# Optimization experiments

Measured on AMD Instinct MI355X. Metric: run time of the kernel, lower is better.

## Reference

```python
import jax, jax.numpy as jnp
import numpy as np

B, SEQ, EMB, HID = 256, 256, 128, 512
NG = 1          # n_glimpses
CEXP = 10.0     # tanh_exploration
NEG = -1e9      # masked-logit value (stands in for -inf)


def setup_inputs():
    key = jax.random.key(0)
    ks = jax.random.split(key, 19)
    se = 1.0 / np.sqrt(EMB)
    sh = 1.0 / np.sqrt(HID)
    u = lambda k, shape, s: jax.random.uniform(k, shape, jnp.float32, -s, s)
    return {
        'embedding': u(ks[0], (SEQ, EMB), 1.0),
        'enc_Wih': u(ks[1], (4 * HID, EMB), sh),
        'enc_Whh': u(ks[2], (4 * HID, HID), sh),
        'enc_b': u(ks[3], (4 * HID,), sh),
        'dec_Wih': u(ks[4], (4 * HID, EMB), sh),
        'dec_Whh': u(ks[5], (4 * HID, HID), sh),
        'dec_b': u(ks[6], (4 * HID,), sh),
        'pt_Wq': u(ks[7], (HID, HID), sh), 'pt_bq': u(ks[8], (HID,), sh),
        'pt_Wref': u(ks[9], (HID, HID), sh), 'pt_bref': u(ks[10], (HID,), sh),
        'pt_V': u(ks[11], (HID,), sh),
        'gl_Wq': u(ks[12], (HID, HID), sh), 'gl_bq': u(ks[13], (HID,), sh),
        'gl_Wref': u(ks[14], (HID, HID), sh), 'gl_bref': u(ks[15], (HID,), sh),
        'gl_V': u(ks[16], (HID,), sh),
        'dec_start': u(ks[17], (EMB,), se),
        'inputs': jax.random.randint(ks[18], (B, SEQ), 0, SEQ),
    }


def lstm_cell(x, h, c, Wih, Whh, b):
    # PyTorch gate order: i, f, g, o
    g = x @ Wih.T + h @ Whh.T + b
    i, f, gg, o = jnp.split(g, 4, axis=1)
    c = jax.nn.sigmoid(f) * c + jax.nn.sigmoid(i) * jnp.tanh(gg)
    h = jax.nn.sigmoid(o) * jnp.tanh(c)
    return h, c


def reference(embedding, enc_Wih, enc_Whh, enc_b,
              dec_Wih, dec_Whh, dec_b,
              pt_Wq, pt_bq, pt_Wref, pt_bref, pt_V,
              gl_Wq, gl_bq, gl_Wref, gl_bref, gl_V,
              dec_start, inputs):
    emb = embedding[inputs]                      # [B,S,E]
    h0 = jnp.zeros((B, HID), jnp.float32)
    c0 = jnp.zeros((B, HID), jnp.float32)

    def enc_step(carry, x_t):
        h, c = carry
        h, c = lstm_cell(x_t, h, c, enc_Wih, enc_Whh, enc_b)
        return (h, c), h

    (h, c), hs = jax.lax.scan(enc_step, (h0, c0), jnp.swapaxes(emb, 0, 1))
    enc_out = jnp.swapaxes(hs, 0, 1)             # [B,S,H]

    # W_ref is a 1x1 Conv1d == per-position linear; precompute once (constant across steps)
    gl_ref = enc_out @ gl_Wref.T + gl_bref       # [B,S,H]
    pt_ref = enc_out @ pt_Wref.T + pt_bref       # [B,S,H]

    keys = jax.random.split(jax.random.key(1), SEQ)
    mask0 = jnp.zeros((B, SEQ), bool)
    dec_in0 = jnp.broadcast_to(dec_start, (B, EMB))

    def dec_step(carry, key_i):
        h, c, mask, dec_in = carry
        h, c = lstm_cell(dec_in, h, c, dec_Wih, dec_Whh, dec_b)
        q = h                                    # [B,H]
        for _ in range(NG):
            gl = jnp.tanh((q @ gl_Wq.T + gl_bq)[:, None, :] + gl_ref) @ gl_V  # [B,S]
            gl = jnp.where(mask, NEG, gl)
            q = jnp.einsum('bsh,bs->bh', gl_ref, jax.nn.softmax(gl, axis=1))
        lg = jnp.tanh((q @ pt_Wq.T + pt_bq)[:, None, :] + pt_ref) @ pt_V      # [B,S]
        lg = CEXP * jnp.tanh(lg)                 # use_tanh=True pointer
        lg = jnp.where(mask, NEG, lg)
        # Categorical sample via Gumbel-max
        gum = -jnp.log(-jnp.log(jax.random.uniform(key_i, (B, SEQ)) + 1e-10) + 1e-10)
        ptr = jnp.argmax(lg + gum, axis=1)       # [B]
        logp = jnp.take_along_axis(jax.nn.log_softmax(lg, axis=1), ptr[:, None], axis=1)[:, 0]
        mask = mask.at[jnp.arange(B), ptr].set(True)
        dec_in = emb[jnp.arange(B), ptr]         # embedding of chosen city
        return (h, c, mask, dec_in), (ptr, logp)

    _, (tours, logps) = jax.lax.scan(dec_step, (h, c, mask0, dec_in0), keys)
    return jnp.swapaxes(tours, 0, 1), jnp.swapaxes(logps, 0, 1)  # [B,S] each
```

## Files before the change

### kernel.cpp

```cpp
#include <hip/hip_runtime.h>
#include <math.h>


#define Bz 256
#define Sz 256
#define Ez 128
#define Hz 512
#define NEGV -1e9f
#define BH (Bz*Hz)

__device__ float g_encout[Bz*Sz*Hz];
__device__ float g_glref[Bz*Sz*Hz];
__device__ float g_ptref[Bz*Sz*Hz];
__device__ float g_xpe[256*2048];
__device__ float g_xpd[257*2048];
__device__ float g_h[2*BH];
__device__ float g_c[BH];
__device__ int g_ptrbuf[Bz];
__device__ unsigned g_keys[2*Sz];
__device__ unsigned char g_mask[Bz*Sz];

__device__ __forceinline__ unsigned rotl32(unsigned v, int d){ return (v<<d)|(v>>(32-d)); }

__device__ __forceinline__ void tf2x32(unsigned k0, unsigned k1, unsigned x0, unsigned x1,
                                       unsigned &o0, unsigned &o1){
  unsigned ks2 = k0 ^ k1 ^ 0x1BD11BDAu;
  x0 += k0; x1 += k1;
#define TFR(r) { x0 += x1; x1 = rotl32(x1,(r)); x1 ^= x0; }
  TFR(13) TFR(15) TFR(26) TFR(6)
  x0 += k1; x1 += ks2 + 1u;
  TFR(17) TFR(29) TFR(16) TFR(24)
  x0 += ks2; x1 += k0 + 2u;
  TFR(13) TFR(15) TFR(26) TFR(6)
  x0 += k0; x1 += k1 + 3u;
  TFR(17) TFR(29) TFR(16) TFR(24)
  x0 += k1; x1 += ks2 + 4u;
  TFR(13) TFR(15) TFR(26) TFR(6)
  x0 += ks2; x1 += k0 + 5u;
#undef TFR
  o0 = x0; o1 = x1;
}

__device__ __forceinline__ unsigned rng_bits(unsigned ka, unsigned kb, unsigned idx){
  unsigned o0,o1; tf2x32(ka,kb, 0u, idx, o0,o1);
  return o0 ^ o1;
}

__global__ __launch_bounds__(256) void init_kernel(){
  int i = blockIdx.x*256 + threadIdx.x;
  if (i < BH){ g_h[i] = 0.f; g_c[i] = 0.f; }
  if (i < Bz*Sz) g_mask[i] = 0;
  if (i < Sz){
    unsigned o0,o1; tf2x32(0u,1u, 0u, (unsigned)i, o0,o1);
    g_keys[2*i] = o0; g_keys[2*i+1] = o1;
  }
}

__global__ __launch_bounds__(256) void xproj_kernel(
    const float* __restrict__ Wih, const float* __restrict__ bias,
    const float* __restrict__ emb, const float* __restrict__ dstart,
    int dst)
{
  float* Xp = dst ? g_xpd : g_xpe;
  int c = blockIdx.x;
  int row = blockIdx.y*256 + threadIdx.x;
  __shared__ float xs[Ez];
  if (threadIdx.x < Ez) xs[threadIdx.x] = (c < 256) ? emb[c*Ez + threadIdx.x]
                                                    : dstart[threadIdx.x];
  __syncthreads();
  float a = bias[row];
  const float* w = Wih + (size_t)row*Ez;
  #pragma unroll 8
  for (int k = 0; k < Ez; k++) a = fmaf(xs[k], w[k], a);
  Xp[(size_t)c*2048 + row] = a;
}

__global__ __launch_bounds__(256) void lstm_step(
    const float* __restrict__ Whh,
    const int*   __restrict__ inputs,
    int t, int is_dec, int hsel)
{
  __shared__ float A_lds[32][36];
  __shared__ float W_lds[64][36];

  const float* h_in = g_h + (size_t)hsel*BH;
  float*       h_out = g_h + (size_t)(hsel^1)*BH;
  const float* Xp = is_dec ? g_xpd : g_xpe;

  int tid = threadIdx.x;
  int bt = blockIdx.x;
  int jt = blockIdx.y;
  int jj = tid & 15;
  int bp = tid >> 4;
  int jglob = jt*16 + jj;

  int bA = bt*32 + bp*2, bB = bA + 1;
  int cA, cB;
  if (is_dec){
    if (t == 0){ cA = 256; cB = 256; }
    else { cA = inputs[bA*Sz + g_ptrbuf[bA]]; cB = inputs[bB*Sz + g_ptrbuf[bB]]; }
  } else {
    cA = inputs[bA*Sz + t]; cB = inputs[bB*Sz + t];
  }

  float acc[2][4];
  {
    const float* xa = Xp + (size_t)cA*2048;
    const float* xb = Xp + (size_t)cB*2048;
    #pragma unroll
    for (int g=0; g<4; g++){
      acc[0][g] = xa[g*Hz + jglob];
      acc[1][g] = xb[g*Hz + jglob];
    }
  }

  int sr = tid >> 3;
  int sk = (tid & 7) * 4;
  int wr = tid >> 2;
  int wk = (tid & 3) * 8;
  int bg = bt*32 + sr;
  int wrow_g = (wr >> 4)*Hz + jt*16 + (wr & 15);

  for (int kc = 0; kc < 16; kc++){
    int k0 = kc*32;
    __syncthreads();
    {
      float4 av = *(const float4*)(h_in + (size_t)bg*Hz + k0 + sk);
      *(float4*)&A_lds[sr][sk] = av;
    }
    {
      const float* ws = Whh + (size_t)wrow_g*Hz + k0 + wk;
      float4 w0 = *(const float4*)ws;
      float4 w1 = *(const float4*)(ws + 4);
      *(float4*)&W_lds[wr][wk]     = w0;
      *(float4*)&W_lds[wr][wk + 4] = w1;
    }
    __syncthreads();
    #pragma unroll
    for (int k4 = 0; k4 < 8; k4++){
      float4 w0 = *(const float4*)&W_lds[jj      ][k4*4];
      float4 w1 = *(const float4*)&W_lds[16 + jj ][k4*4];
      float4 w2 = *(const float4*)&W_lds[32 + jj ][k4*4];
      float4 w3 = *(const float4*)&W_lds[48 + jj ][k4*4];
      float4 a0 = *(const float4*)&A_lds[bp*2    ][k4*4];
      float4 a1 = *(const float4*)&A_lds[bp*2 + 1][k4*4];
#define LSTEP(c) \
      acc[0][0]=fmaf(a0.c,w0.c,acc[0][0]); acc[0][1]=fmaf(a0.c,w1.c,acc[0][1]); \
      acc[0][2]=fmaf(a0.c,w2.c,acc[0][2]); acc[0][3]=fmaf(a0.c,w3.c,acc[0][3]); \
      acc[1][0]=fmaf(a1.c,w0.c,acc[1][0]); acc[1][1]=fmaf(a1.c,w1.c,acc[1][1]); \
      acc[1][2]=fmaf(a1.c,w2.c,acc[1][2]); acc[1][3]=fmaf(a1.c,w3.c,acc[1][3]);
      LSTEP(x) LSTEP(y) LSTEP(z) LSTEP(w)
#undef LSTEP
    }
  }

  #pragma unroll
  for (int r=0;r<2;r++){
    int b = bA + r;
    float gi = acc[r][0], gf = acc[r][1], gg = acc[r][2], go = acc[r][3];
    float co = g_c[(size_t)b*Hz + jglob];
    float si = 1.f/(1.f + expf(-gi));
    float sf = 1.f/(1.f + expf(-gf));
    float so = 1.f/(1.f + expf(-go));
    float cn = sf*co + si*tanhf(gg);
    float hn = so*tanhf(cn);
    g_c[(size_t)b*Hz + jglob] = cn;
    h_out[(size_t)b*Hz + jglob] = hn;
    if (!is_dec) g_encout[((size_t)b*Sz + t)*Hz + jglob] = hn;
  }
}

__global__ __launch_bounds__(256) void gemm_ref(
    const float* __restrict__ W, const float* __restrict__ bias, int dst_id)
{
  const float* A = g_encout;
  float*       C = (dst_id == 1) ? g_glref : g_ptref;
  __shared__ float As[32][68];
  __shared__ float Ws[32][68];
  int tid = threadIdx.x;
  int mt = blockIdx.x * 64, nt = blockIdx.y * 64;
  int tm = (tid & 15) * 4, tn = (tid >> 4) * 4;
  float acc[4][4] = {};
  int lr = tid >> 2;
  int lk = (tid & 3) * 8;

  for (int kc = 0; kc < 16; kc++){
    int k0 = kc*32;
    __syncthreads();
    {
      const float* ar = A + (size_t)(mt + lr)*Hz + k0 + lk;
      float4 a0 = *(const float4*)ar, a1 = *(const float4*)(ar+4);
      As[lk+0][lr]=a0.x; As[lk+1][lr]=a0.y; As[lk+2][lr]=a0.z; As[lk+3][lr]=a0.w;
      As[lk+4][lr]=a1.x; As[lk+5][lr]=a1.y; As[lk+6][lr]=a1.z; As[lk+7][lr]=a1.w;
      const float* wrp = W + (size_t)(nt + lr)*Hz + k0 + lk;
      float4 w0 = *(const float4*)wrp, w1 = *(const float4*)(wrp+4);
      Ws[lk+0][lr]=w0.x; Ws[lk+1][lr]=w0.y; Ws[lk+2][lr]=w0.z; Ws[lk+3][lr]=w0.w;
      Ws[lk+4][lr]=w1.x; Ws[lk+5][lr]=w1.y; Ws[lk+6][lr]=w1.z; Ws[lk+7][lr]=w1.w;
    }
    __syncthreads();
    #pragma unroll
    for (int k=0;k<32;k++){
      float4 av = *(const float4*)&As[k][tm];
      float4 wv = *(const float4*)&Ws[k][tn];
      acc[0][0]=fmaf(av.x,wv.x,acc[0][0]); acc[0][1]=fmaf(av.x,wv.y,acc[0][1]);
      acc[0][2]=fmaf(av.x,wv.z,acc[0][2]); acc[0][3]=fmaf(av.x,wv.w,acc[0][3]);
      acc[1][0]=fmaf(av.y,wv.x,acc[1][0]); acc[1][1]=fmaf(av.y,wv.y,acc[1][1]);
      acc[1][2]=fmaf(av.y,wv.z,acc[1][2]); acc[1][3]=fmaf(av.y,wv.w,acc[1][3]);
      acc[2][0]=fmaf(av.z,wv.x,acc[2][0]); acc[2][1]=fmaf(av.z,wv.y,acc[2][1]);
      acc[2][2]=fmaf(av.z,wv.z,acc[2][2]); acc[2][3]=fmaf(av.z,wv.w,acc[2][3]);
      acc[3][0]=fmaf(av.w,wv.x,acc[3][0]); acc[3][1]=fmaf(av.w,wv.y,acc[3][1]);
      acc[3][2]=fmaf(av.w,wv.z,acc[3][2]); acc[3][3]=fmaf(av.w,wv.w,acc[3][3]);
    }
  }
  float b0v = bias[nt+tn+0], b1v = bias[nt+tn+1], b2v = bias[nt+tn+2], b3v = bias[nt+tn+3];
  #pragma unroll
  for (int i=0;i<4;i++){
    float4 o;
    o.x = acc[i][0] + b0v; o.y = acc[i][1] + b1v;
    o.z = acc[i][2] + b2v; o.w = acc[i][3] + b3v;
    *(float4*)(C + (size_t)(mt + tm + i)*Hz + nt + tn) = o;
  }
}

__global__ __launch_bounds__(512) void attn_step(
    const float* __restrict__ gl_Wq, const float* __restrict__ gl_bq,
    const float* __restrict__ gl_V,
    const float* __restrict__ pt_Wq, const float* __restrict__ pt_bq,
    const float* __restrict__ pt_V,
    int t, int hsel2, float* __restrict__ out)
{
  int b = blockIdx.x, tid = threadIdx.x;
  int wave = tid >> 6, lane64 = tid & 63;
  int g = tid >> 5, lane = tid & 31;

  __shared__ __align__(16) float hq[Hz];
  __shared__ __align__(16) float q2s[Hz];
  __shared__ __align__(16) float qgs[Hz];
  __shared__ __align__(16) float qps[Hz];
  __shared__ __align__(16) float vgl[Hz];
  __shared__ __align__(16) float vpt[Hz];
  __shared__ float part[16][513];
  __shared__ float m_arr[16];
  __shared__ float l_arr[16];
  __shared__ int   rlist[16][16];
  __shared__ float slog[Sz];
  __shared__ float redy[8]; __shared__ int redi[8];
  __shared__ float redm[8]; __shared__ float redsum[8];

  hq[tid]  = g_h[(size_t)hsel2*BH + (size_t)b*Hz + tid];
  vgl[tid] = gl_V[tid];
  vpt[tid] = pt_V[tid];
  __syncthreads();

  const unsigned char* mrow = g_mask + b*Sz;

  int cnt;
  {
    bool un = (lane < 16) ? (mrow[g*16 + lane] == 0) : false;
    unsigned long long bal = __ballot(un);
    unsigned m16 = (unsigned)((g & 1) ? (bal >> 32) : bal) & 0xFFFFu;
    cnt = __popc(m16);
    if (lane < 16){
      if (un){
        int rank = __popc(m16 & ((1u << lane) - 1u));
        rlist[g][rank] = g*16 + lane;
      } else {
        slog[g*16 + lane] = NEGV;
      }
    }
  }

  {
    float hv[8];
    #pragma unroll
    for (int i=0;i<8;i++) hv[i] = hq[lane64*8 + i];
    for (int jj=0;jj<64;jj+=2){
      int j0 = wave*64 + jj;
      const float* wr0 = gl_Wq + (size_t)j0*Hz + lane64*8;
      const float* wr1 = wr0 + Hz;
      float4 A0 = *(const float4*)wr0, A1 = *(const float4*)(wr0+4);
      float4 B0 = *(const float4*)wr1, B1 = *(const float4*)(wr1+4);
      float p0 = 0.f, p1 = 0.f;
      p0 = fmaf(hv[0], A0.x, p0); p0 = fmaf(hv[1], A0.y, p0);
      p0 = fmaf(hv[2], A0.z, p0); p0 = fmaf(hv[3], A0.w, p0);
      p0 = fmaf(hv[4], A1.x, p0); p0 = fmaf(hv[5], A1.y, p0);
      p0 = fmaf(hv[6], A1.z, p0); p0 = fmaf(hv[7], A1.w, p0);
      p1 = fmaf(hv[0], B0.x, p1); p1 = fmaf(hv[1], B0.y, p1);
      p1 = fmaf(hv[2], B0.z, p1); p1 = fmaf(hv[3], B0.w, p1);
      p1 = fmaf(hv[4], B1.x, p1); p1 = fmaf(hv[5], B1.y, p1);
      p1 = fmaf(hv[6], B1.z, p1); p1 = fmaf(hv[7], B1.w, p1);
      #pragma unroll
      for (int off=32; off; off>>=1) p0 += __shfl_xor(p0, off);
      #pragma unroll
      for (int off=32; off; off>>=1) p1 += __shfl_xor(p1, off);
      if (lane64 == 0){ q2s[j0] = p0 + gl_bq[j0]; q2s[j0+1] = p1 + gl_bq[j0+1]; }
    }
  }
  __syncthreads();

  const float* glbase = g_glref + (size_t)b*Sz*Hz;
  {
    float m_g = -INFINITY, l_g = 0.f;
    float4 racc[4];
    { float4 z = {0.f,0.f,0.f,0.f}; racc[0]=z; racc[1]=z; racc[2]=z; racc[3]=z; }

    float4 xn0, xn1, xn2, xn3;
    if (cnt > 0){
      const float4* rp = (const float4*)(glbase + (size_t)rlist[g][0]*Hz);
      xn0 = rp[lane]; xn1 = rp[lane+32]; xn2 = rp[lane+64]; xn3 = rp[lane+96];
    }
    for (int i = 0; i < cnt; i++){
      float4 x0 = xn0, x1 = xn1, x2 = xn2, x3 = xn3;
      if (i + 1 < cnt){
        const float4* rp = (const float4*)(glbase + (size_t)rlist[g][i+1]*Hz);
        xn0 = rp[lane]; xn1 = rp[lane+32]; xn2 = rp[lane+64]; xn3 = rp[lane+96];
      }
      float p = 0.f;
      {
        float4 q, vv;
        q = *(const float4*)&q2s[lane*4];        vv = *(const float4*)&vgl[lane*4];
        p = fmaf(vv.x, tanhf(q.x + x0.x), p); p = fmaf(vv.y, tanhf(q.y + x0.y), p);
        p = fmaf(vv.z, tanhf(q.z + x0.z), p); p = fmaf(vv.w, tanhf(q.w + x0.w), p);
        q = *(const float4*)&q2s[(lane+32)*4];   vv = *(const float4*)&vgl[(lane+32)*4];
        p = fmaf(vv.x, tanhf(q.x + x1.x), p); p = fmaf(vv.y, tanhf(q.y + x1.y), p);
        p = fmaf(vv.z, tanhf(q.z + x1.z), p); p = fmaf(vv.w, tanhf(q.w + x1.w), p);
        q = *(const float4*)&q2s[(lane+64)*4];   vv = *(const float4*)&vgl[(lane+64)*4];
        p = fmaf(vv.x, tanhf(q.x + x2.x), p); p = fmaf(vv.y, tanhf(q.y + x2.y), p);
        p = fmaf(vv.z, tanhf(q.z + x2.z), p); p = fmaf(vv.w, tanhf(q.w + x2.w), p);
        q = *(const float4*)&q2s[(lane+96)*4];   vv = *(const float4*)&vgl[(lane+96)*4];
        p = fmaf(vv.x, tanhf(q.x + x3.x), p); p = fmaf(vv.y, tanhf(q.y + x3.y), p);
        p = fmaf(vv.z, tanhf(q.z + x3.z), p); p = fmaf(vv.w, tanhf(q.w + x3.w), p);
      }
      #pragma unroll
      for (int off=16; off; off>>=1) p += __shfl_xor(p, off, 32);
      float lgv = p;
      if (lgv > m_g){
        float r_ = expf(m_g - lgv);
        l_g *= r_;
        racc[0].x*=r_; racc[0].y*=r_; racc[0].z*=r_; racc[0].w*=r_;
        racc[1].x*=r_; racc[1].y*=r_; racc[1].z*=r_; racc[1].w*=r_;
        racc[2].x*=r_; racc[2].y*=r_; racc[2].z*=r_; racc[2].w*=r_;
        racc[3].x*=r_; racc[3].y*=r_; racc[3].z*=r_; racc[3].w*=r_;
        m_g = lgv;
      }
      float pr = expf(lgv - m_g);
      l_g += pr;
      racc[0].x=fmaf(pr,x0.x,racc[0].x); racc[0].y=fmaf(pr,x0.y,racc[0].y);
      racc[0].z=fmaf(pr,x0.z,racc[0].z); racc[0].w=fmaf(pr,x0.w,racc[0].w);
      racc[1].x=fmaf(pr,x1.x,racc[1].x); racc[1].y=fmaf(pr,x1.y,racc[1].y);
      racc[1].z=fmaf(pr,x1.z,racc[1].z); racc[1].w=fmaf(pr,x1.w,racc[1].w);
      racc[2].x=fmaf(pr,x2.x,racc[2].x); racc[2].y=fmaf(pr,x2.y,racc[2].y);
      racc[2].z=fmaf(pr,x2.z,racc[2].z); racc[2].w=fmaf(pr,x2.w,racc[2].w);
      racc[3].x=fmaf(pr,x3.x,racc[3].x); racc[3].y=fmaf(pr,x3.y,racc[3].y);
      racc[3].z=fmaf(pr,x3.z,racc[3].z); racc[3].w=fmaf(pr,x3.w,racc[3].w);
    }
    if (lane == 0){ m_arr[g] = m_g; l_arr[g] = l_g; }
    part[g][4*lane+  0] = racc[0].x; part[g][4*lane+  1] = racc[0].y;
    part[g][4*lane+  2] = racc[0].z; part[g][4*lane+  3] = racc[0].w;
    part[g][4*lane+128] = racc[1].x; part[g][4*lane+129] = racc[1].y;
    part[g][4*lane+130] = racc[1].z; part[g][4*lane+131] = racc[1].w;
    part[g][4*lane+256] = racc[2].x; part[g][4*lane+257] = racc[2].y;
    part[g][4*lane+258] = racc[2].z; part[g][4*lane+259] = racc[2].w;
    part[g][4*lane+384] = racc[3].x; part[g][4*lane+385] = racc[3].y;
    part[g][4*lane+386] = racc[3].z; part[g][4*lane+387] = racc[3].w;
  }
  __syncthreads();

  {
    float M = m_arr[0];
    #pragma unroll
    for (int gg=1; gg<16; gg++) M = fmaxf(M, m_arr[gg]);
    float num = 0.f, den = 0.f;
    #pragma unroll
    for (int gg=0; gg<16; gg++){
      float w = expf(m_arr[gg] - M);
      num = fmaf(w, part[gg][tid], num);
      den = fmaf(w, l_arr[gg], den);
    }
    qgs[tid] = num / den;
  }
  __syncthreads();

  {
    float qv[8];
    #pragma unroll
    for (int i=0;i<8;i++) qv[i] = qgs[lane64*8 + i];
    for (int jj=0;jj<64;jj+=2){
      int j0 = wave*64 + jj;
      const float* wr0 = pt_Wq + (size_t)j0*Hz + lane64*8;
      const float* wr1 = wr0 + Hz;
      float4 A0 = *(const float4*)wr0, A1 = *(const float4*)(wr0+4);
      float4 B0 = *(const float4*)wr1, B1 = *(const float4*)(wr1+4);
      float p0 = 0.f, p1 = 0.f;
      p0 = fmaf(qv[0], A0.x, p0); p0 = fmaf(qv[1], A0.y, p0);
      p0 = fmaf(qv[2], A0.z, p0); p0 = fmaf(qv[3], A0.w, p0);
      p0 = fmaf(qv[4], A1.x, p0); p0 = fmaf(qv[5], A1.y, p0);
      p0 = fmaf(qv[6], A1.z, p0); p0 = fmaf(qv[7], A1.w, p0);
      p1 = fmaf(qv[0], B0.x, p1); p1 = fmaf(qv[1], B0.y, p1);
      p1 = fmaf(qv[2], B0.z, p1); p1 = fmaf(qv[3], B0.w, p1);
      p1 = fmaf(qv[4], B1.x, p1); p1 = fmaf(qv[5], B1.y, p1);
      p1 = fmaf(qv[6], B1.z, p1); p1 = fmaf(qv[7], B1.w, p1);
      #pragma unroll
      for (int off=32; off; off>>=1) p0 += __shfl_xor(p0, off);
      #pragma unroll
      for (int off=32; off; off>>=1) p1 += __shfl_xor(p1, off);
      if (lane64 == 0){ qps[j0] = p0 + pt_bq[j0]; qps[j0+1] = p1 + pt_bq[j0+1]; }
    }
  }
  __syncthreads();

  const float* ptbase = g_ptref + (size_t)b*Sz*Hz;
  {
    float4 xn0, xn1, xn2, xn3;
    if (cnt > 0){
      const float4* rp = (const float4*)(ptbase + (size_t)rlist[g][0]*Hz);
      xn0 = rp[lane]; xn1 = rp[lane+32]; xn2 = rp[lane+64]; xn3 = rp[lane+96];
    }
    for (int i = 0; i < cnt; i++){
      int s = rlist[g][i];
      float4 x0 = xn0, x1 = xn1, x2 = xn2, x3 = xn3;
      if (i + 1 < cnt){
        const float4* rp = (const float4*)(ptbase + (size_t)rlist[g][i+1]*Hz);
        xn0 = rp[lane]; xn1 = rp[lane+32]; xn2 = rp[lane+64]; xn3 = rp[lane+96];
      }
      float p = 0.f;
      {
        float4 q, vv;
        q = *(const float4*)&qps[lane*4];        vv = *(const float4*)&vpt[lane*4];
        p = fmaf(vv.x, tanhf(q.x + x0.x), p); p = fmaf(vv.y, tanhf(q.y + x0.y), p);
        p = fmaf(vv.z, tanhf(q.z + x0.z), p); p = fmaf(vv.w, tanhf(q.w + x0.w), p);
        q = *(const float4*)&qps[(lane+32)*4];   vv = *(const float4*)&vpt[(lane+32)*4];
        p = fmaf(vv.x, tanhf(q.x + x1.x), p); p = fmaf(vv.y, tanhf(q.y + x1.y), p);
        p = fmaf(vv.z, tanhf(q.z + x1.z), p); p = fmaf(vv.w, tanhf(q.w + x1.w), p);
        q = *(const float4*)&qps[(lane+64)*4];   vv = *(const float4*)&vpt[(lane+64)*4];
        p = fmaf(vv.x, tanhf(q.x + x2.x), p); p = fmaf(vv.y, tanhf(q.y + x2.y), p);
        p = fmaf(vv.z, tanhf(q.z + x2.z), p); p = fmaf(vv.w, tanhf(q.w + x2.w), p);
        q = *(const float4*)&qps[(lane+96)*4];   vv = *(const float4*)&vpt[(lane+96)*4];
        p = fmaf(vv.x, tanhf(q.x + x3.x), p); p = fmaf(vv.y, tanhf(q.y + x3.y), p);
        p = fmaf(vv.z, tanhf(q.z + x3.z), p); p = fmaf(vv.w, tanhf(q.w + x3.w), p);
      }
      #pragma unroll
      for (int off=16; off; off>>=1) p += __shfl_xor(p, off, 32);
      if (lane == 0) slog[s] = 10.f * tanhf(p);
    }
  }
  __syncthreads();

  float lg = NEGV, y = -INFINITY;
  if (tid < Sz){
    lg = slog[tid];
    unsigned bits = rng_bits(g_keys[2*t], g_keys[2*t+1], (unsigned)(b*Sz + tid));
    float u = __uint_as_float((bits >> 9) | 0x3f800000u) - 1.f;
    float gum = -logf(-logf(u + 1e-10f) + 1e-10f);
    y = lg + gum;
  }
  float by = y; int bi = tid; float bm = lg;
  #pragma unroll
  for (int off=32; off; off>>=1){
    float oy = __shfl_xor(by, off);
    int   oi = __shfl_xor(bi, off);
    float om = __shfl_xor(bm, off);
    if (oy > by || (oy == by && oi < bi)){ by = oy; bi = oi; }
    bm = fmaxf(bm, om);
  }
  if (lane64 == 0){ redy[wave] = by; redi[wave] = bi; redm[wave] = bm; }
  __syncthreads();
  float fy = redy[0]; int fi = redi[0]; float fm = redm[0];
  #pragma unroll
  for (int w=1; w<8; w++){
    if (redy[w] > fy || (redy[w] == fy && redi[w] < fi)){ fy = redy[w]; fi = redi[w]; }
    fm = fmaxf(fm, redm[w]);
  }
  int ptr = fi;

  float pe = (tid < Sz) ? expf(lg - fm) : 0.f;
  #pragma unroll
  for (int off=32; off; off>>=1) pe += __shfl_xor(pe, off);
  if (lane64 == 0) redsum[wave] = pe;
  __syncthreads();
  if (tid == 0){
    float den = ((redsum[0]+redsum[1]) + (redsum[2]+redsum[3]))
              + ((redsum[4]+redsum[5]) + (redsum[6]+redsum[7]));
    float logp = slog[ptr] - fm - logf(den);
    out[(size_t)b*Sz + t] = (float)ptr;
    out[(size_t)Bz*Sz + (size_t)b*Sz + t] = logp;
    g_mask[b*Sz + ptr] = 1;
    g_ptrbuf[b] = ptr;
  }
}

extern "C" void kernel_launch(void* const* d_in, const int* in_sizes, int n_in,
                              void* d_out, int out_size, void* d_ws, size_t ws_size,
                              hipStream_t stream){
  (void)in_sizes; (void)n_in; (void)out_size; (void)d_ws; (void)ws_size;
  const float* embedding = (const float*)d_in[0];
  const float* enc_Wih = (const float*)d_in[1];
  const float* enc_Whh = (const float*)d_in[2];
  const float* enc_b   = (const float*)d_in[3];
  const float* dec_Wih = (const float*)d_in[4];
  const float* dec_Whh = (const float*)d_in[5];
  const float* dec_b   = (const float*)d_in[6];
  const float* pt_Wq   = (const float*)d_in[7];
  const float* pt_bq   = (const float*)d_in[8];
  const float* pt_Wref = (const float*)d_in[9];
  const float* pt_bref = (const float*)d_in[10];
  const float* pt_V    = (const float*)d_in[11];
  const float* gl_Wq   = (const float*)d_in[12];
  const float* gl_bq   = (const float*)d_in[13];
  const float* gl_Wref = (const float*)d_in[14];
  const float* gl_bref = (const float*)d_in[15];
  const float* gl_V    = (const float*)d_in[16];
  const float* dec_start = (const float*)d_in[17];
  const int*   inputs  = (const int*)d_in[18];
  float* out = (float*)d_out;

  init_kernel<<<512, 256, 0, stream>>>();
  xproj_kernel<<<dim3(256,8), 256, 0, stream>>>(enc_Wih, enc_b, embedding, dec_start, 0);
  xproj_kernel<<<dim3(257,8), 256, 0, stream>>>(dec_Wih, dec_b, embedding, dec_start, 1);

  for (int t = 0; t < Sz; t++){
    lstm_step<<<dim3(8,32), 256, 0, stream>>>(enc_Whh, inputs, t, 0, t & 1);
  }
  gemm_ref<<<dim3(1024,8), 256, 0, stream>>>(gl_Wref, gl_bref, 1);
  gemm_ref<<<dim3(1024,8), 256, 0, stream>>>(pt_Wref, pt_bref, 2);

  for (int t = 0; t < Sz; t++){
    lstm_step<<<dim3(8,32), 256, 0, stream>>>(dec_Whh, inputs, t, 1, t & 1);
    attn_step<<<Bz, 512, 0, stream>>>(gl_Wq, gl_bq, gl_V,
        pt_Wq, pt_bq, pt_V, t, (t+1) & 1, out);
  }
}
```

Before: 34.79 ms.

## Fuse whole rollout into one persistent cooperative kernel with grid syncs

Replaces the roughly 770 separate kernel launches (init, input projections, per-step encoder and decoder LSTM, reference GEMMs, per-step attention) with one cooperative kernel of 256 blocks × 512 threads. Phases are separated by grid.sync instead of kernel boundaries, and shared memory is held in a union across phases. The LSTM and GEMM tiles are reshaped so each thread in the larger 512-thread block does half the previous work. The aim is to remove per-launch overhead on the sequential recurrence. The cost is grid-wide barrier latency, higher register pressure from one monolithic kernel, and a fixed one-block-per-CU occupancy.

```diff
diff --git a/kernel.cpp b/kernel.cpp
--- a/kernel.cpp
+++ b/kernel.cpp
@@ -1,5 +1,8 @@
 #include <hip/hip_runtime.h>
+#include <hip/hip_cooperative_groups.h>
 #include <math.h>
+
+namespace cg = cooperative_groups;
 
 
 #define Bz 256
@@ -46,210 +49,141 @@
   return o0 ^ o1;
 }
 
-__global__ __launch_bounds__(256) void init_kernel(){
-  int i = blockIdx.x*256 + threadIdx.x;
-  if (i < BH){ g_h[i] = 0.f; g_c[i] = 0.f; }
-  if (i < Bz*Sz) g_mask[i] = 0;
-  if (i < Sz){
-    unsigned o0,o1; tf2x32(0u,1u, 0u, (unsigned)i, o0,o1);
-    g_keys[2*i] = o0; g_keys[2*i+1] = o1;
-  }
-}
-
-__global__ __launch_bounds__(256) void xproj_kernel(
-    const float* __restrict__ Wih, const float* __restrict__ bias,
-    const float* __restrict__ emb, const float* __restrict__ dstart,
-    int dst)
+struct AttnS {
+  float hq[Hz], q2s[Hz], qgs[Hz], qps[Hz], vgl[Hz], vpt[Hz];
+  float part[16][513];
+  float m_arr[16], l_arr[16];
+  int   rlist[16][16];
+  float slog[Sz];
+  float redy[8]; int redi[8]; float redm[8]; float redsum[8];
+};
+struct LstmS { float A[32][36]; float W[64][36]; };
+struct GemmS { float As[32][68]; float Ws[32][68]; };
+struct XprojS { float xs[Ez]; };
+union __align__(16) SharedU { AttnS a; LstmS l; GemmS g; XprojS x; };
+
+__device__ void lstm_phase(LstmS& S, const float* __restrict__ Whh,
+                           const int* __restrict__ inputs,
+                           int t, int is_dec, int hsel, int blk, int tid)
 {
-  float* Xp = dst ? g_xpd : g_xpe;
-  int c = blockIdx.x;
-  int row = blockIdx.y*256 + threadIdx.x;
-  __shared__ float xs[Ez];
-  if (threadIdx.x < Ez) xs[threadIdx.x] = (c < 256) ? emb[c*Ez + threadIdx.x]
-                                                    : dstart[threadIdx.x];
-  __syncthreads();
-  float a = bias[row];
-  const float* w = Wih + (size_t)row*Ez;
-  #pragma unroll 8
-  for (int k = 0; k < Ez; k++) a = fmaf(xs[k], w[k], a);
-  Xp[(size_t)c*2048 + row] = a;
-}
-
-__global__ __launch_bounds__(256) void lstm_step(
-    const float* __restrict__ Whh,
-    const int*   __restrict__ inputs,
-    int t, int is_dec, int hsel)
-{
-  __shared__ float A_lds[32][36];
-  __shared__ float W_lds[64][36];
-
-  const float* h_in = g_h + (size_t)hsel*BH;
+  const float* h_in  = g_h + (size_t)hsel*BH;
   float*       h_out = g_h + (size_t)(hsel^1)*BH;
   const float* Xp = is_dec ? g_xpd : g_xpe;
 
-  int tid = threadIdx.x;
-  int bt = blockIdx.x;
-  int jt = blockIdx.y;
-  int jj = tid & 15;
-  int bp = tid >> 4;
+  int bt = blk >> 5, jt = blk & 31;
+  int jj = tid & 15, bp = tid >> 4;
   int jglob = jt*16 + jj;
-
-  int bA = bt*32 + bp*2, bB = bA + 1;
-  int cA, cB;
-  if (is_dec){
-    if (t == 0){ cA = 256; cB = 256; }
-    else { cA = inputs[bA*Sz + g_ptrbuf[bA]]; cB = inputs[bB*Sz + g_ptrbuf[bB]]; }
-  } else {
-    cA = inputs[bA*Sz + t]; cB = inputs[bB*Sz + t];
-  }
-
-  float acc[2][4];
-  {
-    const float* xa = Xp + (size_t)cA*2048;
-    const float* xb = Xp + (size_t)cB*2048;
-    #pragma unroll
-    for (int g=0; g<4; g++){
-      acc[0][g] = xa[g*Hz + jglob];
-      acc[1][g] = xb[g*Hz + jglob];
-    }
-  }
-
-  int sr = tid >> 3;
+  int b = bt*32 + bp;
+
+  int c;
+  if (is_dec) c = (t == 0) ? 256 : inputs[b*Sz + g_ptrbuf[b]];
+  else        c = inputs[b*Sz + t];
+
+  float acc[4];
+  {
+    const float* xa = Xp + (size_t)c*2048;
+    #pragma unroll
+    for (int g=0; g<4; g++) acc[g] = xa[g*Hz + jglob];
+  }
+
   int sk = (tid & 7) * 4;
-  int wr = tid >> 2;
-  int wk = (tid & 3) * 8;
-  int bg = bt*32 + sr;
+  int wr = tid >> 3;
+  int bgA = bt*32 + (tid >> 3);
   int wrow_g = (wr >> 4)*Hz + jt*16 + (wr & 15);
 
   for (int kc = 0; kc < 16; kc++){
     int k0 = kc*32;
     __syncthreads();
+    if (tid < 256){
+      float4 av = *(const float4*)(h_in + (size_t)bgA*Hz + k0 + sk);
+      *(float4*)&S.A[tid>>3][sk] = av;
+    }
     {
-      float4 av = *(const float4*)(h_in + (size_t)bg*Hz + k0 + sk);
-      *(float4*)&A_lds[sr][sk] = av;
-    }
-    {
-      const float* ws = Whh + (size_t)wrow_g*Hz + k0 + wk;
+      const float* ws = Whh + (size_t)wrow_g*Hz + k0 + sk;
       float4 w0 = *(const float4*)ws;
-      float4 w1 = *(const float4*)(ws + 4);
-      *(float4*)&W_lds[wr][wk]     = w0;
-      *(float4*)&W_lds[wr][wk + 4] = w1;
+      *(float4*)&S.W[wr][sk] = w0;
     }
     __syncthreads();
     #pragma unroll
     for (int k4 = 0; k4 < 8; k4++){
-      float4 w0 = *(const float4*)&W_lds[jj      ][k4*4];
-      float4 w1 = *(const float4*)&W_lds[16 + jj ][k4*4];
-      float4 w2 = *(const float4*)&W_lds[32 + jj ][k4*4];
-      float4 w3 = *(const float4*)&W_lds[48 + jj ][k4*4];
-      float4 a0 = *(const float4*)&A_lds[bp*2    ][k4*4];
-      float4 a1 = *(const float4*)&A_lds[bp*2 + 1][k4*4];
-#define LSTEP(c) \
-      acc[0][0]=fmaf(a0.c,w0.c,acc[0][0]); acc[0][1]=fmaf(a0.c,w1.c,acc[0][1]); \
-      acc[0][2]=fmaf(a0.c,w2.c,acc[0][2]); acc[0][3]=fmaf(a0.c,w3.c,acc[0][3]); \
-      acc[1][0]=fmaf(a1.c,w0.c,acc[1][0]); acc[1][1]=fmaf(a1.c,w1.c,acc[1][1]); \
-      acc[1][2]=fmaf(a1.c,w2.c,acc[1][2]); acc[1][3]=fmaf(a1.c,w3.c,acc[1][3]);
+      float4 w0 = *(const float4*)&S.W[jj      ][k4*4];
+      float4 w1 = *(const float4*)&S.W[16 + jj ][k4*4];
+      float4 w2 = *(const float4*)&S.W[32 + jj ][k4*4];
+      float4 w3 = *(const float4*)&S.W[48 + jj ][k4*4];
+      float4 a0 = *(const float4*)&S.A[bp][k4*4];
+#define LSTEP(c_) \
+      acc[0]=fmaf(a0.c_,w0.c_,acc[0]); acc[1]=fmaf(a0.c_,w1.c_,acc[1]); \
+      acc[2]=fmaf(a0.c_,w2.c_,acc[2]); acc[3]=fmaf(a0.c_,w3.c_,acc[3]);
       LSTEP(x) LSTEP(y) LSTEP(z) LSTEP(w)
 #undef LSTEP
     }
   }
 
-  #pragma unroll
-  for (int r=0;r<2;r++){
-    int b = bA + r;
-    float gi = acc[r][0], gf = acc[r][1], gg = acc[r][2], go = acc[r][3];
-    float co = g_c[(size_t)b*Hz + jglob];
-    float si = 1.f/(1.f + expf(-gi));
-    float sf = 1.f/(1.f + expf(-gf));
-    float so = 1.f/(1.f + expf(-go));
-    float cn = sf*co + si*tanhf(gg);
-    float hn = so*tanhf(cn);
-    g_c[(size_t)b*Hz + jglob] = cn;
-    h_out[(size_t)b*Hz + jglob] = hn;
-    if (!is_dec) g_encout[((size_t)b*Sz + t)*Hz + jglob] = hn;
-  }
-}
-
-__global__ __launch_bounds__(256) void gemm_ref(
-    const float* __restrict__ W, const float* __restrict__ bias, int dst_id)
+  float gi = acc[0], gf = acc[1], gg = acc[2], go = acc[3];
+  float co = g_c[(size_t)b*Hz + jglob];
+  float si = 1.f/(1.f + expf(-gi));
+  float sf = 1.f/(1.f + expf(-gf));
+  float so = 1.f/(1.f + expf(-go));
+  float cn = sf*co + si*tanhf(gg);
+  float hn = so*tanhf(cn);
+  g_c[(size_t)b*Hz + jglob] = cn;
+  h_out[(size_t)b*Hz + jglob] = hn;
+  if (!is_dec) g_encout[((size_t)b*Sz + t)*Hz + jglob] = hn;
+}
+
+__device__ void gemm_tile(GemmS& S, const float* __restrict__ W,
+                          const float* __restrict__ bias, float* __restrict__ C,
+                          int mt, int nt, int tid)
 {
   const float* A = g_encout;
-  float*       C = (dst_id == 1) ? g_glref : g_ptref;
-  __shared__ float As[32][68];
-  __shared__ float Ws[32][68];
-  int tid = threadIdx.x;
-  int mt = blockIdx.x * 64, nt = blockIdx.y * 64;
-  int tm = (tid & 15) * 4, tn = (tid >> 4) * 4;
-  float acc[4][4] = {};
-  int lr = tid >> 2;
-  int lk = (tid & 3) * 8;
+  int tm = (tid & 15) * 4, tn = (tid >> 4) * 2;
+  float acc[4][2] = {};
+  int lr = tid >> 3;
+  int lk = (tid & 7) * 4;
 
   for (int kc = 0; kc < 16; kc++){
     int k0 = kc*32;
     __syncthreads();
     {
       const float* ar = A + (size_t)(mt + lr)*Hz + k0 + lk;
-      float4 a0 = *(const float4*)ar, a1 = *(const float4*)(ar+4);
-      As[lk+0][lr]=a0.x; As[lk+1][lr]=a0.y; As[lk+2][lr]=a0.z; As[lk+3][lr]=a0.w;
-      As[lk+4][lr]=a1.x; As[lk+5][lr]=a1.y; As[lk+6][lr]=a1.z; As[lk+7][lr]=a1.w;
+      float4 a0 = *(const float4*)ar;
+      S.As[lk+0][lr]=a0.x; S.As[lk+1][lr]=a0.y; S.As[lk+2][lr]=a0.z; S.As[lk+3][lr]=a0.w;
       const float* wrp = W + (size_t)(nt + lr)*Hz + k0 + lk;
-      float4 w0 = *(const float4*)wrp, w1 = *(const float4*)(wrp+4);
-      Ws[lk+0][lr]=w0.x; Ws[lk+1][lr]=w0.y; Ws[lk+2][lr]=w0.z; Ws[lk+3][lr]=w0.w;
-      Ws[lk+4][lr]=w1.x; Ws[lk+5][lr]=w1.y; Ws[lk+6][lr]=w1.z; Ws[lk+7][lr]=w1.w;
+      float4 w0 = *(const float4*)wrp;
+      S.Ws[lk+0][lr]=w0.x; S.Ws[lk+1][lr]=w0.y; S.Ws[lk+2][lr]=w0.z; S.Ws[lk+3][lr]=w0.w;
     }
     __syncthreads();
     #pragma unroll
     for (int k=0;k<32;k++){
-      float4 av = *(const float4*)&As[k][tm];
-      float4 wv = *(const float4*)&Ws[k][tn];
+      float4 av = *(const float4*)&S.As[k][tm];
+      float2 wv = *(const float2*)&S.Ws[k][tn];
       acc[0][0]=fmaf(av.x,wv.x,acc[0][0]); acc[0][1]=fmaf(av.x,wv.y,acc[0][1]);
-      acc[0][2]=fmaf(av.x,wv.z,acc[0][2]); acc[0][3]=fmaf(av.x,wv.w,acc[0][3]);
       acc[1][0]=fmaf(av.y,wv.x,acc[1][0]); acc[1][1]=fmaf(av.y,wv.y,acc[1][1]);
-      acc[1][2]=fmaf(av.y,wv.z,acc[1][2]); acc[1][3]=fmaf(av.y,wv.w,acc[1][3]);
       acc[2][0]=fmaf(av.z,wv.x,acc[2][0]); acc[2][1]=fmaf(av.z,wv.y,acc[2][1]);
-      acc[2][2]=fmaf(av.z,wv.z,acc[2][2]); acc[2][3]=fmaf(av.z,wv.w,acc[2][3]);
       acc[3][0]=fmaf(av.w,wv.x,acc[3][0]); acc[3][1]=fmaf(av.w,wv.y,acc[3][1]);
-      acc[3][2]=fmaf(av.w,wv.z,acc[3][2]); acc[3][3]=fmaf(av.w,wv.w,acc[3][3]);
-    }
-  }
-  float b0v = bias[nt+tn+0], b1v = bias[nt+tn+1], b2v = bias[nt+tn+2], b3v = bias[nt+tn+3];
+    }
+  }
+  float b0v = bias[nt+tn+0], b1v = bias[nt+tn+1];
   #pragma unroll
   for (int i=0;i<4;i++){
-    float4 o;
-    o.x = acc[i][0] + b0v; o.y = acc[i][1] + b1v;
-    o.z = acc[i][2] + b2v; o.w = acc[i][3] + b3v;
-    *(float4*)(C + (size_t)(mt + tm + i)*Hz + nt + tn) = o;
-  }
-}
-
-__global__ __launch_bounds__(512) void attn_step(
+    float2 o; o.x = acc[i][0] + b0v; o.y = acc[i][1] + b1v;
+    *(float2*)(C + (size_t)(mt + tm + i)*Hz + nt + tn) = o;
+  }
+}
+
+__device__ void attn_phase(AttnS& S,
     const float* __restrict__ gl_Wq, const float* __restrict__ gl_bq,
     const float* __restrict__ gl_V,
     const float* __restrict__ pt_Wq, const float* __restrict__ pt_bq,
     const float* __restrict__ pt_V,
-    int t, int hsel2, float* __restrict__ out)
+    int t, int hsel2, float* __restrict__ out, int b, int tid)
 {
-  int b = blockIdx.x, tid = threadIdx.x;
   int wave = tid >> 6, lane64 = tid & 63;
   int g = tid >> 5, lane = tid & 31;
 
-  __shared__ __align__(16) float hq[Hz];
-  __shared__ __align__(16) float q2s[Hz];
-  __shared__ __align__(16) float qgs[Hz];
-  __shared__ __align__(16) float qps[Hz];
-  __shared__ __align__(16) float vgl[Hz];
-  __shared__ __align__(16) float vpt[Hz];
-  __shared__ float part[16][513];
-  __shared__ float m_arr[16];
-  __shared__ float l_arr[16];
-  __shared__ int   rlist[16][16];
-  __shared__ float slog[Sz];
-  __shared__ float redy[8]; __shared__ int redi[8];
-  __shared__ float redm[8]; __shared__ float redsum[8];
-
-  hq[tid]  = g_h[(size_t)hsel2*BH + (size_t)b*Hz + tid];
-  vgl[tid] = gl_V[tid];
-  vpt[tid] = pt_V[tid];
+  S.hq[tid]  = g_h[(size_t)hsel2*BH + (size_t)b*Hz + tid];
+  S.vgl[tid] = gl_V[tid];
+  S.vpt[tid] = pt_V[tid];
   __syncthreads();
 
   const unsigned char* mrow = g_mask + b*Sz;
@@ -263,9 +197,9 @@
     if (lane < 16){
       if (un){
         int rank = __popc(m16 & ((1u << lane) - 1u));
-        rlist[g][rank] = g*16 + lane;
+        S.rlist[g][rank] = g*16 + lane;
       } else {
-        slog[g*16 + lane] = NEGV;
+        S.slog[g*16 + lane] = NEGV;
       }
     }
   }
@@ -273,7 +207,7 @@
   {
     float hv[8];
     #pragma unroll
-    for (int i=0;i<8;i++) hv[i] = hq[lane64*8 + i];
+    for (int i=0;i<8;i++) hv[i] = S.hq[lane64*8 + i];
     for (int jj=0;jj<64;jj+=2){
       int j0 = wave*64 + jj;
       const float* wr0 = gl_Wq + (size_t)j0*Hz + lane64*8;
@@ -293,7 +227,7 @@
       for (int off=32; off; off>>=1) p0 += __shfl_xor(p0, off);
       #pragma unroll
       for (int off=32; off; off>>=1) p1 += __shfl_xor(p1, off);
-      if (lane64 == 0){ q2s[j0] = p0 + gl_bq[j0]; q2s[j0+1] = p1 + gl_bq[j0+1]; }
+      if (lane64 == 0){ S.q2s[j0] = p0 + gl_bq[j0]; S.q2s[j0+1] = p1 + gl_bq[j0+1]; }
     }
   }
   __syncthreads();
@@ -306,28 +240,28 @@
 
     float4 xn0, xn1, xn2, xn3;
     if (cnt > 0){
-      const float4* rp = (const float4*)(glbase + (size_t)rlist[g][0]*Hz);
+      const float4* rp = (const float4*)(glbase + (size_t)S.rlist[g][0]*Hz);
       xn0 = rp[lane]; xn1 = rp[lane+32]; xn2 = rp[lane+64]; xn3 = rp[lane+96];
     }
     for (int i = 0; i < cnt; i++){
       float4 x0 = xn0, x1 = xn1, x2 = xn2, x3 = xn3;
       if (i + 1 < cnt){
-        const float4* rp = (const float4*)(glbase + (size_t)rlist[g][i+1]*Hz);
+        const float4* rp = (const float4*)(glbase + (size_t)S.rlist[g][i+1]*Hz);
         xn0 = rp[lane]; xn1 = rp[lane+32]; xn2 = rp[lane+64]; xn3 = rp[lane+96];
       }
       float p = 0.f;
       {
         float4 q, vv;
-        q = *(const float4*)&q2s[lane*4];        vv = *(const float4*)&vgl[lane*4];
+        q = *(const float4*)&S.q2s[lane*4];        vv = *(const float4*)&S.vgl[lane*4];
         p = fmaf(vv.x, tanhf(q.x + x0.x), p); p = fmaf(vv.y, tanhf(q.y + x0.y), p);
         p = fmaf(vv.z, tanhf(q.z + x0.z), p); p = fmaf(vv.w, tanhf(q.w + x0.w), p);
-        q = *(const float4*)&q2s[(lane+32)*4];   vv = *(const float4*)&vgl[(lane+32)*4];
+        q = *(const float4*)&S.q2s[(lane+32)*4];   vv = *(const float4*)&S.vgl[(lane+32)*4];
         p = fmaf(vv.x, tanhf(q.x + x1.x), p); p = fmaf(vv.y, tanhf(q.y + x1.y), p);
         p = fmaf(vv.z, tanhf(q.z + x1.z), p); p = fmaf(vv.w, tanhf(q.w + x1.w), p);
-        q = *(const float4*)&q2s[(lane+64)*4];   vv = *(const float4*)&vgl[(lane+64)*4];
+        q = *(const float4*)&S.q2s[(lane+64)*4];   vv = *(const float4*)&S.vgl[(lane+64)*4];
         p = fmaf(vv.x, tanhf(q.x + x2.x), p); p = fmaf(vv.y, tanhf(q.y + x2.y), p);
         p = fmaf(vv.z, tanhf(q.z + x2.z), p); p = fmaf(vv.w, tanhf(q.w + x2.w), p);
-        q = *(const float4*)&q2s[(lane+96)*4];   vv = *(const float4*)&vgl[(lane+96)*4];
+        q = *(const float4*)&S.q2s[(lane+96)*4];   vv = *(const float4*)&S.vgl[(lane+96)*4];
         p = fmaf(vv.x, tanhf(q.x + x3.x), p); p = fmaf(vv.y, tanhf(q.y + x3.y), p);
         p = fmaf(vv.z, tanhf(q.z + x3.z), p); p = fmaf(vv.w, tanhf(q.w + x3.w), p);
       }
@@ -354,37 +288,37 @@
       racc[3].x=fmaf(pr,x3.x,racc[3].x); racc[3].y=fmaf(pr,x3.y,racc[3].y);
       racc[3].z=fmaf(pr,x3.z,racc[3].z); racc[3].w=fmaf(pr,x3.w,racc[3].w);
     }
-    if (lane == 0){ m_arr[g] = m_g; l_arr[g] = l_g; }
-    part[g][4*lane+  0] = racc[0].x; part[g][4*lane+  1] = racc[0].y;
-    part[g][4*lane+  2] = racc[0].z; part[g][4*lane+  3] = racc[0].w;
-    part[g][4*lane+128] = racc[1].x; part[g][4*lane+129] = racc[1].y;
-    part[g][4*lane+130] = racc[1].z; part[g][4*lane+131] = racc[1].w;
-    part[g][4*lane+256] = racc[2].x; part[g][4*lane+257] = racc[2].y;
-    part[g][4*lane+258] = racc[2].z; part[g][4*lane+259] = racc[2].w;
-    part[g][4*lane+384] = racc[3].x; part[g][4*lane+385] = racc[3].y;
-    part[g][4*lane+386] = racc[3].z; part[g][4*lane+387] = racc[3].w;
-  }
-  __syncthreads();
-
-  {
-    float M = m_arr[0];
-    #pragma unroll
-    for (int gg=1; gg<16; gg++) M = fmaxf(M, m_arr[gg]);
+    if (lane == 0){ S.m_arr[g] = m_g; S.l_arr[g] = l_g; }
+    S.part[g][4*lane+  0] = racc[0].x; S.part[g][4*lane+  1] = racc[0].y;
+    S.part[g][4*lane+  2] = racc[0].z; S.part[g][4*lane+  3] = racc[0].w;
+    S.part[g][4*lane+128] = racc[1].x; S.part[g][4*lane+129] = racc[1].y;
+    S.part[g][4*lane+130] = racc[1].z; S.part[g][4*lane+131] = racc[1].w;
+    S.part[g][4*lane+256] = racc[2].x; S.part[g][4*lane+257] = racc[2].y;
+    S.part[g][4*lane+258] = racc[2].z; S.part[g][4*lane+259] = racc[2].w;
+    S.part[g][4*lane+384] = racc[3].x; S.part[g][4*lane+385] = racc[3].y;
+    S.part[g][4*lane+386] = racc[3].z; S.part[g][4*lane+387] = racc[3].w;
+  }
+  __syncthreads();
+
+  {
+    float M = S.m_arr[0];
+    #pragma unroll
+    for (int gg=1; gg<16; gg++) M = fmaxf(M, S.m_arr[gg]);
     float num = 0.f, den = 0.f;
     #pragma unroll
     for (int gg=0; gg<16; gg++){
-      float w = expf(m_arr[gg] - M);
-      num = fmaf(w, part[gg][tid], num);
-      den = fmaf(w, l_arr[gg], den);
-    }
-    qgs[tid] = num / den;
+      float w = expf(S.m_arr[gg] - M);
+      num = fmaf(w, S.part[gg][tid], num);
+      den = fmaf(w, S.l_arr[gg], den);
+    }
+    S.qgs[tid] = num / den;
   }
   __syncthreads();
 
   {
     float qv[8];
     #pragma unroll
-    for (int i=0;i<8;i++) qv[i] = qgs[lane64*8 + i];
+    for (int i=0;i<8;i++) qv[i] = S.qgs[lane64*8 + i];
     for (int jj=0;jj<64;jj+=2){
       int j0 = wave*64 + jj;
       const float* wr0 = pt_Wq + (size_t)j0*Hz + lane64*8;
@@ -404,7 +338,7 @@
       for (int off=32; off; off>>=1) p0 += __shfl_xor(p0, off);
       #pragma unroll
       for (int off=32; off; off>>=1) p1 += __shfl_xor(p1, off);
-      if (lane64 == 0){ qps[j0] = p0 + pt_bq[j0]; qps[j0+1] = p1 + pt_bq[j0+1]; }
+      if (lane64 == 0){ S.qps[j0] = p0 + pt_bq[j0]; S.qps[j0+1] = p1 + pt_bq[j0+1]; }
     }
   }
   __syncthreads();
@@ -413,42 +347,42 @@
   {
     float4 xn0, xn1, xn2, xn3;
     if (cnt > 0){
-      const float4* rp = (const float4*)(ptbase + (size_t)rlist[g][0]*Hz);
+      const float4* rp = (const float4*)(ptbase + (size_t)S.rlist[g][0]*Hz);
       xn0 = rp[lane]; xn1 = rp[lane+32]; xn2 = rp[lane+64]; xn3 = rp[lane+96];
     }
     for (int i = 0; i < cnt; i++){
-      int s = rlist[g][i];
+      int s = S.rlist[g][i];
       float4 x0 = xn0, x1 = xn1, x2 = xn2, x3 = xn3;
       if (i + 1 < cnt){
-        const float4* rp = (const float4*)(ptbase + (size_t)rlist[g][i+1]*Hz);
+        const float4* rp = (const float4*)(ptbase + (size_t)S.rlist[g][i+1]*Hz);
         xn0 = rp[lane]; xn1 = rp[lane+32]; xn2 = rp[lane+64]; xn3 = rp[lane+96];
       }
       float p = 0.f;
       {
         float4 q, vv;
-        q = *(const float4*)&qps[lane*4];        vv = *(const float4*)&vpt[lane*4];
+        q = *(const float4*)&S.qps[lane*4];        vv = *(const float4*)&S.vpt[lane*4];
         p = fmaf(vv.x, tanhf(q.x + x0.x), p); p = fmaf(vv.y, tanhf(q.y + x0.y), p);
         p = fmaf(vv.z, tanhf(q.z + x0.z), p); p = fmaf(vv.w, tanhf(q.w + x0.w), p);
-        q = *(const float4*)&qps[(lane+32)*4];   vv = *(const float4*)&vpt[(lane+32)*4];
+        q = *(const float4*)&S.qps[(lane+32)*4];   vv = *(const float4*)&S.vpt[(lane+32)*4];
         p = fmaf(vv.x, tanhf(q.x + x1.x), p); p = fmaf(vv.y, tanhf(q.y + x1.y), p);
         p = fmaf(vv.z, tanhf(q.z + x1.z), p); p = fmaf(vv.w, tanhf(q.w + x1.w), p);
-        q = *(const float4*)&qps[(lane+64)*4];   vv = *(const float4*)&vpt[(lane+64)*4];
+        q = *(const float4*)&S.qps[(lane+64)*4];   vv = *(const float4*)&S.vpt[(lane+64)*4];
         p = fmaf(vv.x, tanhf(q.x + x2.x), p); p = fmaf(vv.y, tanhf(q.y + x2.y), p);
         p = fmaf(vv.z, tanhf(q.z + x2.z), p); p = fmaf(vv.w, tanhf(q.w + x2.w), p);
-        q = *(const float4*)&qps[(lane+96)*4];   vv = *(const float4*)&vpt[(lane+96)*4];
+        q = *(const float4*)&S.qps[(lane+96)*4];   vv = *(const float4*)&S.vpt[(lane+96)*4];
         p = fmaf(vv.x, tanhf(q.x + x3.x), p); p = fmaf(vv.y, tanhf(q.y + x3.y), p);
         p = fmaf(vv.z, tanhf(q.z + x3.z), p); p = fmaf(vv.w, tanhf(q.w + x3.w), p);
       }
       #pragma unroll
       for (int off=16; off; off>>=1) p += __shfl_xor(p, off, 32);
-      if (lane == 0) slog[s] = 10.f * tanhf(p);
+      if (lane == 0) S.slog[s] = 10.f * tanhf(p);
     }
   }
   __syncthreads();
 
   float lg = NEGV, y = -INFINITY;
   if (tid < Sz){
-    lg = slog[tid];
+    lg = S.slog[tid];
     unsigned bits = rng_bits(g_keys[2*t], g_keys[2*t+1], (unsigned)(b*Sz + tid));
     float u = __uint_as_float((bits >> 9) | 0x3f800000u) - 1.f;
     float gum = -logf(-logf(u + 1e-10f) + 1e-10f);
@@ -463,29 +397,93 @@
     if (oy > by || (oy == by && oi < bi)){ by = oy; bi = oi; }
     bm = fmaxf(bm, om);
   }
-  if (lane64 == 0){ redy[wave] = by; redi[wave] = bi; redm[wave] = bm; }
-  __syncthreads();
-  float fy = redy[0]; int fi = redi[0]; float fm = redm[0];
+  if (lane64 == 0){ S.redy[wave] = by; S.redi[wave] = bi; S.redm[wave] = bm; }
+  __syncthreads();
+  float fy = S.redy[0]; int fi = S.redi[0]; float fm = S.redm[0];
   #pragma unroll
   for (int w=1; w<8; w++){
-    if (redy[w] > fy || (redy[w] == fy && redi[w] < fi)){ fy = redy[w]; fi = redi[w]; }
-    fm = fmaxf(fm, redm[w]);
+    if (S.redy[w] > fy || (S.redy[w] == fy && S.redi[w] < fi)){ fy = S.redy[w]; fi = S.redi[w]; }
+    fm = fmaxf(fm, S.redm[w]);
   }
   int ptr = fi;
 
   float pe = (tid < Sz) ? expf(lg - fm) : 0.f;
   #pragma unroll
   for (int off=32; off; off>>=1) pe += __shfl_xor(pe, off);
-  if (lane64 == 0) redsum[wave] = pe;
+  if (lane64 == 0) S.redsum[wave] = pe;
   __syncthreads();
   if (tid == 0){
-    float den = ((redsum[0]+redsum[1]) + (redsum[2]+redsum[3]))
-              + ((redsum[4]+redsum[5]) + (redsum[6]+redsum[7]));
-    float logp = slog[ptr] - fm - logf(den);
+    float den = ((S.redsum[0]+S.redsum[1]) + (S.redsum[2]+S.redsum[3]))
+              + ((S.redsum[4]+S.redsum[5]) + (S.redsum[6]+S.redsum[7]));
+    float logp = S.slog[ptr] - fm - logf(den);
     out[(size_t)b*Sz + t] = (float)ptr;
     out[(size_t)Bz*Sz + (size_t)b*Sz + t] = logp;
     g_mask[b*Sz + ptr] = 1;
     g_ptrbuf[b] = ptr;
+  }
+}
+
+__global__ void __launch_bounds__(512)
+rollout_kernel(const float* embedding, const float* enc_Wih, const float* enc_Whh,
+  const float* enc_b, const float* dec_Wih, const float* dec_Whh, const float* dec_b,
+  const float* pt_Wq, const float* pt_bq, const float* pt_Wref, const float* pt_bref,
+  const float* pt_V, const float* gl_Wq, const float* gl_bq, const float* gl_Wref,
+  const float* gl_bref, const float* gl_V, const float* dec_start, const int* inputs,
+  float* out)
+{
+  cg::grid_group grid = cg::this_grid();
+  __shared__ SharedU sh;
+  int blk = blockIdx.x, tid = threadIdx.x;
+
+  {
+    int i = blk*512 + tid;
+    if (i < BH){ g_h[i] = 0.f; g_c[i] = 0.f; }
+    if (i < Bz*Sz) g_mask[i] = 0;
+    if (i < Sz){
+      unsigned o0,o1; tf2x32(0u,1u, 0u, (unsigned)i, o0,o1);
+      g_keys[2*i] = o0; g_keys[2*i+1] = o1;
+    }
+  }
+
+  for (int tile = blk; tile < 2052; tile += 256){
+    int is_dec = tile >= 1024;
+    int idx = is_dec ? tile - 1024 : tile;
+    int c = idx >> 2, chunk = idx & 3;
+    const float* Wih  = is_dec ? dec_Wih : enc_Wih;
+    const float* bias = is_dec ? dec_b   : enc_b;
+    float* Xp = is_dec ? g_xpd : g_xpe;
+    __syncthreads();
+    if (tid < Ez) sh.x.xs[tid] = (c < 256) ? embedding[c*Ez + tid] : dec_start[tid];
+    __syncthreads();
+    int row = chunk*512 + tid;
+    float a = bias[row];
+    const float* w = Wih + (size_t)row*Ez;
+    #pragma unroll 8
+    for (int k = 0; k < Ez; k++) a = fmaf(sh.x.xs[k], w[k], a);
+    Xp[(size_t)c*2048 + row] = a;
+  }
+  grid.sync();
+
+  for (int t = 0; t < Sz; t++){
+    lstm_phase(sh.l, enc_Whh, inputs, t, 0, t & 1, blk, tid);
+    grid.sync();
+  }
+
+  for (int tile = blk; tile < 16384; tile += 256){
+    int sel = tile >> 13;
+    int mt = ((tile & 8191) >> 3) * 64;
+    int nt = (tile & 7) * 64;
+    if (sel == 0) gemm_tile(sh.g, gl_Wref, gl_bref, g_glref, mt, nt, tid);
+    else          gemm_tile(sh.g, pt_Wref, pt_bref, g_ptref, mt, nt, tid);
+  }
+  grid.sync();
+
+  for (int t = 0; t < Sz; t++){
+    lstm_phase(sh.l, dec_Whh, inputs, t, 1, t & 1, blk, tid);
+    grid.sync();
+    attn_phase(sh.a, gl_Wq, gl_bq, gl_V, pt_Wq, pt_bq, pt_V,
+               t, (t+1) & 1, out, blk, tid);
+    grid.sync();
   }
 }
 
@@ -514,19 +512,13 @@
   const int*   inputs  = (const int*)d_in[18];
   float* out = (float*)d_out;
 
-  init_kernel<<<512, 256, 0, stream>>>();
-  xproj_kernel<<<dim3(256,8), 256, 0, stream>>>(enc_Wih, enc_b, embedding, dec_start, 0);
-  xproj_kernel<<<dim3(257,8), 256, 0, stream>>>(dec_Wih, dec_b, embedding, dec_start, 1);
-
-  for (int t = 0; t < Sz; t++){
-    lstm_step<<<dim3(8,32), 256, 0, stream>>>(enc_Whh, inputs, t, 0, t & 1);
-  }
-  gemm_ref<<<dim3(1024,8), 256, 0, stream>>>(gl_Wref, gl_bref, 1);
-  gemm_ref<<<dim3(1024,8), 256, 0, stream>>>(pt_Wref, pt_bref, 2);
-
-  for (int t = 0; t < Sz; t++){
-    lstm_step<<<dim3(8,32), 256, 0, stream>>>(dec_Whh, inputs, t, 1, t & 1);
-    attn_step<<<Bz, 512, 0, stream>>>(gl_Wq, gl_bq, gl_V,
-        pt_Wq, pt_bq, pt_V, t, (t+1) & 1, out);
-  }
-}
+  void* args[] = {
+    (void*)&embedding, (void*)&enc_Wih, (void*)&enc_Whh, (void*)&enc_b,
+    (void*)&dec_Wih, (void*)&dec_Whh, (void*)&dec_b,
+    (void*)&pt_Wq, (void*)&pt_bq, (void*)&pt_Wref, (void*)&pt_bref, (void*)&pt_V,
+    (void*)&gl_Wq, (void*)&gl_bq, (void*)&gl_Wref, (void*)&gl_bref, (void*)&gl_V,
+    (void*)&dec_start, (void*)&inputs, (void*)&out
+  };
+  hipLaunchCooperativeKernel((void*)rollout_kernel, dim3(256), dim3(512),
+                             args, 0, stream);
+}
```

Measured after the change: 61.40 ms. 76.5% more time.
